# Performance work log

Hardware: AMD Instinct MI355X
Metric: run time of the kernel (lower is better)

Reference implementation:

```python
import jax, jax.numpy as jnp
import numpy as np

B, N, E, F, H = 8, 20000, 640000, 8, 128


def setup_inputs() -> dict:
    key = jax.random.key(0)
    ks = jax.random.split(key, 8)
    x = jax.random.normal(ks[0], (B, N, F), dtype=jnp.float32)
    edge_index = jax.random.randint(ks[1], (B, 2, E), 0, N, dtype=jnp.int64)
    node_idx = jax.random.randint(ks[2], (B,), 0, N, dtype=jnp.int64)
    W1 = jax.random.normal(ks[3], (F, H), dtype=jnp.float32) / np.sqrt(F)
    W2 = jax.random.normal(ks[4], (H, H), dtype=jnp.float32) / np.sqrt(H)
    W3 = jax.random.normal(ks[5], (H, H), dtype=jnp.float32) / np.sqrt(H)
    Wl = jax.random.normal(ks[6], (H, 2), dtype=jnp.float32) / np.sqrt(H)
    return {
        "x": x, "edge_index": edge_index, "node_idx": node_idx,
        "W1": W1, "b1": jnp.zeros((H,), jnp.float32),
        "W2": W2, "b2": jnp.zeros((H,), jnp.float32),
        "W3": W3, "b3": jnp.zeros((H,), jnp.float32),
        "Wl": Wl, "bl": jnp.zeros((2,), jnp.float32),
    }


def _gcn_conv(x, edge_index, W, b):
    # PyG GCNConv: h = x W; out = D^{-1/2}(A+I)D^{-1/2} h + b  (self-loops added)
    n = x.shape[0]
    h = x @ W  # [N, H]
    src, dst = edge_index[0], edge_index[1]
    ones = jnp.ones(src.shape[0], dtype=x.dtype)
    deg = jax.ops.segment_sum(ones, dst, num_segments=n) + 1.0  # +1 for self-loop
    dinv = jax.lax.rsqrt(deg)  # [N]
    coef = dinv[src] * dinv[dst]  # [E]
    agg = jax.ops.segment_sum(h[src] * coef[:, None], dst, num_segments=n)
    agg = agg + h * (dinv * dinv)[:, None]  # self-loop contribution
    return agg + b


def _per_graph(x, edge_index, node_idx, W1, b1, W2, b2, W3, b3, Wl, bl):
    h = jax.nn.relu(_gcn_conv(x, edge_index, W1, b1))
    h = jax.nn.relu(h @ W2 + b2)
    h = jax.nn.relu(h @ W3 + b3)
    # dropout is identity in eval mode
    logits = h @ Wl + bl  # [N, 2]
    return logits[node_idx].flatten()  # [2]


def reference(x, edge_index, node_idx, W1, b1, W2, b2, W3, b3, Wl, bl):
    f = jax.vmap(_per_graph, in_axes=(0, 0, 0, None, None, None, None, None, None, None, None))
    return f(x, edge_index, node_idx, W1, b1, W2, b2, W3, b3, Wl, bl)  # [B, 2]
```

## Files before the change

kernel.cpp:

```cpp
#include <hip/hip_runtime.h>

#define NB 8
#define NN 20000
#define NE 640000
#define NF 8
#define NH 128
#define VPG (NE / 4)
#define WPG 64
#define NBLK (NB * WPG)
#define CHUNK_V (VPG / WPG)
#define SLOT 32
#define HW (NN / 4)
#define CAP 256
#define CAP1 (CAP + 1)

#define FLAGA_MAG 0x5A7BC0DEull
#define FLAGB_VAL 0xD00DFEEDC0FFEE42ull

#define WS_FLAGA_OFF 0
#define WS_FLAGB_OFF (NBLK * 8)
#define WS_LSTA_OFF  (WS_FLAGB_OFF + NBLK * 8)
#define WS_DEGP_OFF  (WS_LSTA_OFF + NBLK * SLOT * 4)

__device__ __forceinline__ void st32a(int* p, int v) {
    __hip_atomic_store(p, v, __ATOMIC_RELAXED, __HIP_MEMORY_SCOPE_AGENT);
}
__device__ __forceinline__ int ld32a(int* p) {
    return __hip_atomic_load(p, __ATOMIC_RELAXED, __HIP_MEMORY_SCOPE_AGENT);
}
__device__ __forceinline__ void st64a(unsigned long long* p, unsigned long long v) {
    __hip_atomic_store(p, v, __ATOMIC_RELAXED, __HIP_MEMORY_SCOPE_AGENT);
}
__device__ __forceinline__ unsigned long long ld64a(unsigned long long* p) {
    return __hip_atomic_load(p, __ATOMIC_RELAXED, __HIP_MEMORY_SCOPE_AGENT);
}

__global__ __launch_bounds__(256) void fused_gcn(
    const float* __restrict__ x, const int* __restrict__ ei,
    const int* __restrict__ nidx,
    const float* __restrict__ W1, const float* __restrict__ b1,
    const float* __restrict__ W2, const float* __restrict__ b2,
    const float* __restrict__ W3, const float* __restrict__ b3,
    const float* __restrict__ Wl, const float* __restrict__ bl,
    unsigned long long* __restrict__ flagA, unsigned long long* __restrict__ flagB,
    int* __restrict__ lstA, int* __restrict__ degp,
    float* __restrict__ out)
{
    const int tid  = threadIdx.x;
    const int lane = tid & 63, wv = tid >> 6;

    __shared__ unsigned histo[HW];
    __shared__ int wtot[4];
    __shared__ int carr[WPG], coff[WPG];
    __shared__ int ntot;
    __shared__ int compact[CAP];
    __shared__ int degT[CAP1];
    __shared__ float dinv[CAP1];
    __shared__ float pp[2 * NH];
    __shared__ float h1[NH], h2[NH], h3[NH];

    if (blockIdx.x < NBLK) {
        const int bid = blockIdx.x, b = bid / WPG, w = bid % WPG;
        const int bbase = b * WPG;
        const int tgt = nidx[b];
        const int* dstp = ei + (size_t)b * 2 * NE + NE;
        const int* srcp = ei + (size_t)b * 2 * NE;
        const int start = w * CHUNK_V;

        for (int i = tid; i < HW; i += 256) histo[i] = 0u;
        __syncthreads();

        unsigned long long mmask = 0ull;
        {
            int it = 0;
            for (int v = start + tid; v < start + CHUNK_V; v += 256, ++it) {
                int4 d = ((const int4*)dstp)[v];
                int dd[4] = {d.x, d.y, d.z, d.w};
                unsigned m4 = 0u;
#pragma unroll
                for (int c = 0; c < 4; ++c) {
                    atomicAdd(&histo[dd[c] >> 2], 1u << ((dd[c] & 3) * 8));
                    m4 |= (dd[c] == tgt ? 1u : 0u) << c;
                }
                mmask |= (unsigned long long)m4 << (it * 4);
            }
        }
        const int mycnt = __popcll(mmask);
        int v = mycnt;
#pragma unroll
        for (int d = 1; d < 64; d <<= 1) {
            int o = __shfl_up(v, d, 64);
            if (lane >= d) v += o;
        }
        if (lane == 63) wtot[wv] = v;
        __syncthreads();
        int wo = 0;
        for (int i = 0; i < wv; ++i) wo += wtot[i];
        {
            int base = v + wo - mycnt;
            unsigned long long mm = mmask;
            while (mm) {
                int bit = __ffsll(mm) - 1; mm &= mm - 1;
                int it2 = bit >> 2, c = bit & 3;
                int e = 4 * (start + tid + it2 * 256) + c;
                if (base < SLOT) st32a(&lstA[(bbase + w) * SLOT + base], srcp[e]);
                ++base;
            }
        }
        int mtot = wtot[0] + wtot[1] + wtot[2] + wtot[3];
        if (mtot > SLOT) mtot = SLOT;
        asm volatile("s_waitcnt vmcnt(0)" ::: "memory");
        __syncthreads();
        if (tid == 0)
            st64a(&flagA[bbase + w], (FLAGA_MAG << 32) | (unsigned)mtot);

        if (tid < WPG) {
            unsigned long long f;
            while (((f = ld64a(&flagA[bbase + tid])) >> 32) != FLAGA_MAG)
                __builtin_amdgcn_s_sleep(2);
            carr[tid] = (int)(f & 0xFFFFFFFFull);
        }
        if (tid < WPG) {
            int cv = carr[tid];
            int s = cv;
#pragma unroll
            for (int d = 1; d < WPG; d <<= 1) {
                int o = __shfl_up(s, d, 64);
                if (lane >= d) s += o;
            }
            coff[tid] = s - cv;
            if (tid == WPG - 1) ntot = s;
        }
        __syncthreads();
        int n = ntot; if (n > CAP) n = CAP;
        for (int idx = tid; idx < WPG * SLOT; idx += 256) {
            int w2 = idx >> 5, s = idx & 31;
            if (s < carr[w2]) {
                int pos = coff[w2] + s;
                if (pos < CAP) compact[pos] = ld32a(&lstA[(bbase + w2) * SLOT + s]);
            }
        }
        __syncthreads();
        for (int i = tid; i <= n; i += 256) {
            int node = (i == n) ? tgt : compact[i];
            unsigned pw = histo[node >> 2];
            int dgr = (int)((pw >> ((node & 3) * 8)) & 0xFFu);
            st32a(&degp[((size_t)b * CAP1 + i) * WPG + w], dgr);
        }
        asm volatile("s_waitcnt vmcnt(0)" ::: "memory");
        __syncthreads();
        if (tid == 0) st64a(&flagB[bbase + w], FLAGB_VAL);
        return;
    }

    const int b = blockIdx.x - NBLK;
    const int bbase = b * WPG;
    const int tgt = nidx[b];

    if (tid < WPG) {
        unsigned long long f;
        while (((f = ld64a(&flagA[bbase + tid])) >> 32) != FLAGA_MAG)
            __builtin_amdgcn_s_sleep(2);
        carr[tid] = (int)(f & 0xFFFFFFFFull);
    }
    if (tid < WPG) {
        int cv = carr[tid];
        int s = cv;
#pragma unroll
        for (int d = 1; d < WPG; d <<= 1) {
            int o = __shfl_up(s, d, 64);
            if (lane >= d) s += o;
        }
        coff[tid] = s - cv;
        if (tid == WPG - 1) ntot = s;
    }
    __syncthreads();
    int n = ntot; if (n > CAP) n = CAP;
    for (int idx = tid; idx < WPG * SLOT; idx += 256) {
        int w2 = idx >> 5, s = idx & 31;
        if (s < carr[w2]) {
            int pos = coff[w2] + s;
            if (pos < CAP) compact[pos] = ld32a(&lstA[(bbase + w2) * SLOT + s]);
        }
    }
    if (tid < WPG) {
        while (ld64a(&flagB[bbase + tid]) != FLAGB_VAL)
            __builtin_amdgcn_s_sleep(2);
    }
    __syncthreads();
    for (int i = tid; i <= n; i += 256) degT[i] = 0;
    __syncthreads();
    for (int idx = tid; idx < (n + 1) * 2; idx += 256) {
        int i = idx >> 1, g = idx & 1;
        int* row = &degp[((size_t)b * CAP1 + i) * WPG];
        int s = 0;
#pragma unroll
        for (int k = 0; k < 32; ++k) s += ld32a(&row[g * 32 + k]);
        atomicAdd(&degT[i], s);
    }
    __syncthreads();
    for (int i = tid; i <= n; i += 256)
        dinv[i] = rsqrtf((float)(degT[i] + 1));
    __syncthreads();

    const float* xb = x + (size_t)b * NN * NF;
    const float dt = dinv[n];
    const int j = tid & (NH - 1);
    const int half = tid >> 7;

    {
        float acc = 0.f;
        for (int i = half; i <= n; i += 2) {
            int s = (i == n) ? tgt : compact[i];
            float coef = (i == n) ? dt * dt : dinv[i] * dt;
            const float* xs = xb + (size_t)s * NF;
            float hs = 0.f;
#pragma unroll
            for (int k = 0; k < NF; ++k) hs += xs[k] * W1[k * NH + j];
            acc += hs * coef;
        }
        pp[half * NH + j] = acc;
    }
    __syncthreads();
    if (tid < NH) { float v1 = pp[j] + pp[NH + j] + b1[j]; h1[j] = v1 > 0.f ? v1 : 0.f; }
    __syncthreads();
    {
        float a = 0.f;
        const int k0 = half * 64;
#pragma unroll 8
        for (int k = k0; k < k0 + 64; ++k) a += h1[k] * W2[k * NH + j];
        pp[half * NH + j] = a;
    }
    __syncthreads();
    if (tid < NH) { float v2 = pp[j] + pp[NH + j] + b2[j]; h2[j] = v2 > 0.f ? v2 : 0.f; }
    __syncthreads();
    {
        float a = 0.f;
        const int k0 = half * 64;
#pragma unroll 8
        for (int k = k0; k < k0 + 64; ++k) a += h2[k] * W3[k * NH + j];
        pp[half * NH + j] = a;
    }
    __syncthreads();
    if (tid < NH) { float v3 = pp[j] + pp[NH + j] + b3[j]; h3[j] = v3 > 0.f ? v3 : 0.f; }
    __syncthreads();
    if (tid < 2) {
        float o = bl[tid];
        for (int k = 0; k < NH; ++k) o += h3[k] * Wl[k * 2 + tid];
        out[b * 2 + tid] = o;
    }
}

extern "C" void kernel_launch(void* const* d_in, const int* in_sizes, int n_in,
                              void* d_out, int out_size, void* d_ws, size_t ws_size,
                              hipStream_t stream) {
    const float* x    = (const float*)d_in[0];
    const int*   ei   = (const int*)d_in[1];
    const int*   nidx = (const int*)d_in[2];
    const float* W1 = (const float*)d_in[3];
    const float* b1 = (const float*)d_in[4];
    const float* W2 = (const float*)d_in[5];
    const float* b2 = (const float*)d_in[6];
    const float* W3 = (const float*)d_in[7];
    const float* b3 = (const float*)d_in[8];
    const float* Wl = (const float*)d_in[9];
    const float* bl = (const float*)d_in[10];
    float* out = (float*)d_out;

    char* ws = (char*)d_ws;
    unsigned long long* flagA = (unsigned long long*)(ws + WS_FLAGA_OFF);
    unsigned long long* flagB = (unsigned long long*)(ws + WS_FLAGB_OFF);
    int* lstA = (int*)(ws + WS_LSTA_OFF);
    int* degp = (int*)(ws + WS_DEGP_OFF);

    fused_gcn<<<NBLK + NB, 256, 0, stream>>>(x, ei, nidx, W1, b1, W2, b2,
                                             W3, b3, Wl, bl,
                                             flagA, flagB, lstA, degp, out);
}
```

Before: 24.27 us.

## Double edge-scan blocks per graph to 128 and rework count scan

Raises the number of edge-scanning blocks per graph from 64 to 128, which halves each block's chunk and cuts per-block slot capacity to 16. The 64-lane prefix scan over per-block counts becomes a two-wave scan, degree partial reduction uses four groups per node, and node indices are clamped for safety. The aim is more parallelism in the histogram and match scan, at the cost of more blocks, more flags to poll and a larger degree-partials reduction.

```diff
diff --git a/kernel.cpp b/kernel.cpp
--- a/kernel.cpp
+++ b/kernel.cpp
@@ -6,10 +6,10 @@
 #define NF 8
 #define NH 128
 #define VPG (NE / 4)
-#define WPG 64
+#define WPG 128
 #define NBLK (NB * WPG)
 #define CHUNK_V (VPG / WPG)
-#define SLOT 32
+#define SLOT 16
 #define HW (NN / 4)
 #define CAP 256
 #define CAP1 (CAP + 1)
@@ -70,7 +70,7 @@
         for (int i = tid; i < HW; i += 256) histo[i] = 0u;
         __syncthreads();
 
-        unsigned long long mmask = 0ull;
+        unsigned mmask = 0u;
         {
             int it = 0;
             for (int v = start + tid; v < start + CHUNK_V; v += 256, ++it) {
@@ -82,10 +82,10 @@
                     atomicAdd(&histo[dd[c] >> 2], 1u << ((dd[c] & 3) * 8));
                     m4 |= (dd[c] == tgt ? 1u : 0u) << c;
                 }
-                mmask |= (unsigned long long)m4 << (it * 4);
-            }
-        }
-        const int mycnt = __popcll(mmask);
+                mmask |= m4 << (it * 4);
+            }
+        }
+        const int mycnt = __popc(mmask);
         int v = mycnt;
 #pragma unroll
         for (int d = 1; d < 64; d <<= 1) {
@@ -98,9 +98,9 @@
         for (int i = 0; i < wv; ++i) wo += wtot[i];
         {
             int base = v + wo - mycnt;
-            unsigned long long mm = mmask;
+            unsigned mm = mmask;
             while (mm) {
-                int bit = __ffsll(mm) - 1; mm &= mm - 1;
+                int bit = __ffs(mm) - 1; mm &= mm - 1;
                 int it2 = bit >> 2, c = bit & 3;
                 int e = 4 * (start + tid + it2 * 256) + c;
                 if (base < SLOT) st32a(&lstA[(bbase + w) * SLOT + base], srcp[e]);
@@ -120,21 +120,28 @@
                 __builtin_amdgcn_s_sleep(2);
             carr[tid] = (int)(f & 0xFFFFFFFFull);
         }
+        __syncthreads();
+        int cv = 0, sincl = 0;
         if (tid < WPG) {
-            int cv = carr[tid];
-            int s = cv;
-#pragma unroll
-            for (int d = 1; d < WPG; d <<= 1) {
-                int o = __shfl_up(s, d, 64);
-                if (lane >= d) s += o;
-            }
-            coff[tid] = s - cv;
-            if (tid == WPG - 1) ntot = s;
+            cv = carr[tid];
+            sincl = cv;
+#pragma unroll
+            for (int d = 1; d < 64; d <<= 1) {
+                int o = __shfl_up(sincl, d, 64);
+                if (lane >= d) sincl += o;
+            }
+            if (lane == 63) wtot[wv] = sincl;
+        }
+        __syncthreads();
+        if (tid < WPG) {
+            int prev = (wv >= 1) ? wtot[0] : 0;
+            coff[tid] = sincl - cv + prev;
+            if (tid == WPG - 1) ntot = sincl + prev;
         }
         __syncthreads();
         int n = ntot; if (n > CAP) n = CAP;
         for (int idx = tid; idx < WPG * SLOT; idx += 256) {
-            int w2 = idx >> 5, s = idx & 31;
+            int w2 = idx / SLOT, s = idx % SLOT;
             if (s < carr[w2]) {
                 int pos = coff[w2] + s;
                 if (pos < CAP) compact[pos] = ld32a(&lstA[(bbase + w2) * SLOT + s]);
@@ -143,6 +150,7 @@
         __syncthreads();
         for (int i = tid; i <= n; i += 256) {
             int node = (i == n) ? tgt : compact[i];
+            node = ((unsigned)node < NN) ? node : 0;
             unsigned pw = histo[node >> 2];
             int dgr = (int)((pw >> ((node & 3) * 8)) & 0xFFu);
             st32a(&degp[((size_t)b * CAP1 + i) * WPG + w], dgr);
@@ -157,27 +165,35 @@
     const int bbase = b * WPG;
     const int tgt = nidx[b];
 
+    for (int i = tid; i < CAP; i += 256) compact[i] = 0;
     if (tid < WPG) {
         unsigned long long f;
         while (((f = ld64a(&flagA[bbase + tid])) >> 32) != FLAGA_MAG)
             __builtin_amdgcn_s_sleep(2);
         carr[tid] = (int)(f & 0xFFFFFFFFull);
     }
-    if (tid < WPG) {
-        int cv = carr[tid];
-        int s = cv;
-#pragma unroll
-        for (int d = 1; d < WPG; d <<= 1) {
-            int o = __shfl_up(s, d, 64);
-            if (lane >= d) s += o;
-        }
-        coff[tid] = s - cv;
-        if (tid == WPG - 1) ntot = s;
+    __syncthreads();
+    int cv = 0, sincl = 0;
+    if (tid < WPG) {
+        cv = carr[tid];
+        sincl = cv;
+#pragma unroll
+        for (int d = 1; d < 64; d <<= 1) {
+            int o = __shfl_up(sincl, d, 64);
+            if (lane >= d) sincl += o;
+        }
+        if (lane == 63) wtot[wv] = sincl;
+    }
+    __syncthreads();
+    if (tid < WPG) {
+        int prev = (wv >= 1) ? wtot[0] : 0;
+        coff[tid] = sincl - cv + prev;
+        if (tid == WPG - 1) ntot = sincl + prev;
     }
     __syncthreads();
     int n = ntot; if (n > CAP) n = CAP;
     for (int idx = tid; idx < WPG * SLOT; idx += 256) {
-        int w2 = idx >> 5, s = idx & 31;
+        int w2 = idx / SLOT, s = idx % SLOT;
         if (s < carr[w2]) {
             int pos = coff[w2] + s;
             if (pos < CAP) compact[pos] = ld32a(&lstA[(bbase + w2) * SLOT + s]);
@@ -190,8 +206,8 @@
     __syncthreads();
     for (int i = tid; i <= n; i += 256) degT[i] = 0;
     __syncthreads();
-    for (int idx = tid; idx < (n + 1) * 2; idx += 256) {
-        int i = idx >> 1, g = idx & 1;
+    for (int idx = tid; idx < (n + 1) * 4; idx += 256) {
+        int i = idx >> 2, g = idx & 3;
         int* row = &degp[((size_t)b * CAP1 + i) * WPG];
         int s = 0;
 #pragma unroll
@@ -212,6 +228,7 @@
         float acc = 0.f;
         for (int i = half; i <= n; i += 2) {
             int s = (i == n) ? tgt : compact[i];
+            s = ((unsigned)s < NN) ? s : 0;
             float coef = (i == n) ? dt * dt : dinv[i] * dt;
             const float* xs = xb + (size_t)s * NF;
             float hs = 0.f;
```

Result: slower. 30.07 us (+23.9%).
